# Optimization experiments

Hardware: AMD Instinct MI355X
Metric: run time of the kernel (lower is better)

## Reference

```python
import jax, jax.numpy as jnp
import numpy as np
import math

B, L, D, H = 4, 2048, 1024, 16
DH = D // H


def setup_inputs() -> dict:
    key = jax.random.key(0)
    ks = jax.random.split(key, 12)
    s = 0.02
    q = jax.random.normal(ks[0], (B, L, D), jnp.float32)
    k = jax.random.normal(ks[1], (B, L, D), jnp.float32)
    v = jax.random.normal(ks[2], (B, L, D), jnp.float32)
    # realistic padding: each sequence has a valid prefix of length in [L//2, L]
    lengths = jax.random.randint(ks[3], (B,), L // 2, L + 1)
    attention_mask = jnp.arange(L)[None, :] < lengths[:, None]  # [B, L] bool
    Wq = jax.random.normal(ks[4], (D, D), jnp.float32) * s
    bq = jnp.zeros((D,), jnp.float32)
    Wk = jax.random.normal(ks[5], (D, D), jnp.float32) * s
    bk = jnp.zeros((D,), jnp.float32)
    Wv = jax.random.normal(ks[6], (D, D), jnp.float32) * s
    bv = jnp.zeros((D,), jnp.float32)
    Wc = jax.random.normal(ks[7], (D, D), jnp.float32) * s
    bc = jnp.zeros((D,), jnp.float32)
    return {"q": q, "k": k, "v": v, "attention_mask": attention_mask,
            "Wq": Wq, "bq": bq, "Wk": Wk, "bk": bk,
            "Wv": Wv, "bv": bv, "Wc": Wc, "bc": bc}


def reference(q, k, v, attention_mask, Wq, bq, Wk, bk, Wv, bv, Wc, bc):
    b, l, d = q.shape
    # projections -> [B, H, L, DH]
    wq = (q @ Wq.T + bq).reshape(b, l, H, DH).transpose(0, 2, 1, 3)
    wk = (k @ Wk.T + bk).reshape(b, l, H, DH).transpose(0, 2, 1, 3)
    wv = (v @ Wv.T + bv).reshape(b, l, H, DH).transpose(0, 2, 1, 3)
    scores = jnp.einsum('bhqd,bhkd->bhqk', wq, wk) / math.sqrt(DH)  # [B,H,L,L]
    # fused causal + padding mask (additive, finfo.min like the torch code)
    pad2d = attention_mask[:, :, None] & attention_mask[:, None, :]  # [B,L,L]
    causal = jnp.tril(jnp.ones((l, l), dtype=bool))
    mask = pad2d[:, None, :, :] & causal[None, None, :, :]  # [B,1,L,L] -> broadcast over heads
    min_val = jnp.finfo(scores.dtype).min
    scores = scores + jnp.where(mask, jnp.float32(0.0), min_val).astype(scores.dtype)
    att = jax.nn.softmax(scores, axis=-1)
    out = jnp.einsum('bhqk,bhkd->bhqd', att, wv)  # [B,H,L,DH]
    out = out.transpose(0, 2, 1, 3).reshape(b, l, H * DH)
    return out @ Wc.T + bc
```

## Files before the change

### kernel.cpp

```cpp
#include <hip/hip_runtime.h>
#include <stdint.h>

typedef __bf16 bf16x8 __attribute__((ext_vector_type(8)));
typedef float f32x4 __attribute__((ext_vector_type(4)));
typedef unsigned short ushort8 __attribute__((ext_vector_type(8)));
typedef unsigned short ushort4v __attribute__((ext_vector_type(4)));

constexpr int CB = 4;
constexpr int CL = 2048;
constexpr int CD = 1024;
constexpr int CH = 16;
constexpr int CDH = 64;
constexpr int CM = CB * CL;

__device__ __forceinline__ unsigned short f2bf(float f) {
  union { float f; unsigned u; } x; x.f = f;
  unsigned r = x.u + 0x7fffu + ((x.u >> 16) & 1u);
  return (unsigned short)(r >> 16);
}
__device__ __forceinline__ float bf2f(unsigned short b) {
  union { unsigned u; float f; } x; x.u = ((unsigned)b) << 16;
  return x.f;
}

__device__ __forceinline__ void gld_lds16(const void* g, void* l) {
  __builtin_amdgcn_global_load_lds((const __attribute__((address_space(1))) void*)g,
                                   (__attribute__((address_space(3))) void*)l, 16, 0, 0);
}

#define MFMA16(a, b, c) __builtin_amdgcn_mfma_f32_16x16x32_bf16((a), (b), (c), 0, 0, 0)


__global__ __launch_bounds__(256) void cvt3_kernel(const float* __restrict__ q,
                                                   const float* __restrict__ k,
                                                   const float* __restrict__ v,
                                                   unsigned short* __restrict__ oq,
                                                   unsigned short* __restrict__ ok,
                                                   unsigned short* __restrict__ ov) {
  const int which = blockIdx.x >> 12;
  const int i = (blockIdx.x & 4095) * 256 + threadIdx.x;
  const float* s = which == 0 ? q : which == 1 ? k : v;
  unsigned short* d = which == 0 ? oq : which == 1 ? ok : ov;
  const float4* sp = (const float4*)s;
  float4 a = sp[2 * i], b = sp[2 * i + 1];
  ushort8 o;
  o[0] = f2bf(a.x); o[1] = f2bf(a.y); o[2] = f2bf(a.z); o[3] = f2bf(a.w);
  o[4] = f2bf(b.x); o[5] = f2bf(b.y); o[6] = f2bf(b.z); o[7] = f2bf(b.w);
  ((ushort8*)d)[i] = o;
}

__global__ __launch_bounds__(256) void cvtw_kernel(const float* w0, const float* w1,
                                                   const float* w2, const float* w3,
                                                   unsigned short* o0, unsigned short* o1,
                                                   unsigned short* o2, unsigned short* o3) {
  const int which = blockIdx.x >> 9;
  const int i = (blockIdx.x & 511) * 256 + threadIdx.x;
  const float* s = which == 0 ? w0 : which == 1 ? w1 : which == 2 ? w2 : w3;
  unsigned short* d = which == 0 ? o0 : which == 1 ? o1 : which == 2 ? o2 : o3;
  const float4* sp = (const float4*)s;
  float4 a = sp[2 * i], b = sp[2 * i + 1];
  ushort8 o;
  o[0] = f2bf(a.x); o[1] = f2bf(a.y); o[2] = f2bf(a.z); o[3] = f2bf(a.w);
  o[4] = f2bf(b.x); o[5] = f2bf(b.y); o[6] = f2bf(b.z); o[7] = f2bf(b.w);
  ((ushort8*)d)[i] = o;
}


__global__ __launch_bounds__(256) void lens_kernel(const int* __restrict__ mask,
                                                   int* __restrict__ lens) {
  __shared__ int part[4];
  const int b = blockIdx.x;
  int cnt = 0;
  for (int i = threadIdx.x; i < CL; i += 256) cnt += (mask[b * CL + i] != 0) ? 1 : 0;
#pragma unroll
  for (int off = 32; off; off >>= 1) cnt += __shfl_down(cnt, off);
  if ((threadIdx.x & 63) == 0) part[threadIdx.x >> 6] = cnt;
  __syncthreads();
  if (threadIdx.x == 0) lens[b] = part[0] + part[1] + part[2] + part[3];
}


__global__ __launch_bounds__(512) void gemm_qkv(const unsigned short* __restrict__ Xq,
                                                const unsigned short* __restrict__ Xk,
                                                const unsigned short* __restrict__ Xv,
                                                const unsigned short* __restrict__ Wb,
                                                const float* __restrict__ bq,
                                                const float* __restrict__ bk,
                                                const float* __restrict__ bv,
                                                unsigned short* __restrict__ Qp,
                                                unsigned short* __restrict__ Kp,
                                                unsigned short* __restrict__ Vt,
                                                float qscale) {
  __shared__ unsigned short Asm[2][128 * 32];
  __shared__ unsigned short Bsm[2][128 * 32];
  const int tid = threadIdx.x;
  const int w = tid >> 6, ln = tid & 63, lr = ln & 15, lq = ln >> 4;
  const int nbx = 24;
  const int cpx = (int)gridDim.x >> 3;
  const int bid = ((int)blockIdx.x & 7) * cpx + ((int)blockIdx.x >> 3);
  const int bm = (bid / nbx) << 7;
  const int bnG = (bid % nbx) << 7;
  const int which = bnG >> 10, bn = bnG & 1023;
  const unsigned short* A = which == 0 ? Xq : which == 1 ? Xk : Xv;
  const unsigned short* Bw = Wb + ((size_t)which << 20);
  const float* bias = which == 0 ? bq : which == 1 ? bk : bv;
  const float alpha = which == 0 ? qscale : 1.0f;
  const int wr = (w >> 1) << 5, wc = (w & 1) << 6;

  f32x4 acc[2][4] = {};
  const int arow = tid >> 2, akc = (tid & 3) << 3;

  auto stage = [&](int buf, int k0) {
    gld_lds16(A + (size_t)(bm + arow) * CD + k0 + akc, (void*)(Asm[buf] + w * 512));
    gld_lds16(Bw + (size_t)(bn + arow) * CD + k0 + akc, (void*)(Bsm[buf] + w * 512));
  };

  stage(0, 0);
  __syncthreads();

  const int nkt = CD >> 5;
  for (int kt = 0; kt < nkt; ++kt) {
    const int cur = kt & 1;
    if (kt + 1 < nkt) stage(cur ^ 1, (kt + 1) << 5);
    bf16x8 af[2], bfr[4];
#pragma unroll
    for (int f = 0; f < 2; ++f)
      af[f] = *(const bf16x8*)(Asm[cur] + ((wr + f * 16 + lr) * 32 + lq * 8));
#pragma unroll
    for (int f = 0; f < 4; ++f)
      bfr[f] = *(const bf16x8*)(Bsm[cur] + ((wc + f * 16 + lr) * 32 + lq * 8));
#pragma unroll
    for (int fm = 0; fm < 2; ++fm)
#pragma unroll
      for (int fn = 0; fn < 4; ++fn)
        acc[fm][fn] = MFMA16(af[fm], bfr[fn], acc[fm][fn]);
    __syncthreads();
  }

#pragma unroll
  for (int fm = 0; fm < 2; ++fm) {
    const int row0 = bm + wr + fm * 16 + lq * 4;
#pragma unroll
    for (int fn = 0; fn < 4; ++fn) {
      const int col = bn + wc + fn * 16 + lr;
      const float bb = bias[col];
      if (which == 2) {
        const int b = row0 >> 11, lrow = row0 & (CL - 1);
        const int hh = col >> 6, dh = col & 63;
        ushort4v pk;
#pragma unroll
        for (int j = 0; j < 4; ++j) pk[j] = f2bf(acc[fm][fn][j] + bb);
        *(ushort4v*)(Vt + (((size_t)((b * CH + hh) * CDH + dh)) << 11) + lrow) = pk;
      } else {
        unsigned short* outp = which == 0 ? Qp : Kp;
#pragma unroll
        for (int j = 0; j < 4; ++j)
          outp[(size_t)(row0 + j) * CD + col] = f2bf((acc[fm][fn][j] + bb) * alpha);
      }
    }
  }
}


__global__ __launch_bounds__(512) void gemm_out(const unsigned short* __restrict__ A,
                                                const unsigned short* __restrict__ Bw,
                                                const float* __restrict__ bias,
                                                float* __restrict__ Cout) {
  __shared__ unsigned short Asm[2][128 * 32];
  __shared__ unsigned short Bsm[2][128 * 32];
  const int tid = threadIdx.x;
  const int w = tid >> 6, ln = tid & 63, lr = ln & 15, lq = ln >> 4;
  const int nbx = CD >> 7;
  const int cpx = (int)gridDim.x >> 3;
  const int bid = ((int)blockIdx.x & 7) * cpx + ((int)blockIdx.x >> 3);
  const int bm = (bid / nbx) << 7;
  const int bn = (bid % nbx) << 7;
  const int wr = (w >> 1) << 5, wc = (w & 1) << 6;

  f32x4 acc[2][4] = {};
  const int arow = tid >> 2, akc = (tid & 3) << 3;

  auto stage = [&](int buf, int k0) {
    gld_lds16(A + (size_t)(bm + arow) * CD + k0 + akc, (void*)(Asm[buf] + w * 512));
    gld_lds16(Bw + (size_t)(bn + arow) * CD + k0 + akc, (void*)(Bsm[buf] + w * 512));
  };

  stage(0, 0);
  __syncthreads();

  const int nkt = CD >> 5;
  for (int kt = 0; kt < nkt; ++kt) {
    const int cur = kt & 1;
    if (kt + 1 < nkt) stage(cur ^ 1, (kt + 1) << 5);
    bf16x8 af[2], bfr[4];
#pragma unroll
    for (int f = 0; f < 2; ++f)
      af[f] = *(const bf16x8*)(Asm[cur] + ((wr + f * 16 + lr) * 32 + lq * 8));
#pragma unroll
    for (int f = 0; f < 4; ++f)
      bfr[f] = *(const bf16x8*)(Bsm[cur] + ((wc + f * 16 + lr) * 32 + lq * 8));
#pragma unroll
    for (int fm = 0; fm < 2; ++fm)
#pragma unroll
      for (int fn = 0; fn < 4; ++fn)
        acc[fm][fn] = MFMA16(af[fm], bfr[fn], acc[fm][fn]);
    __syncthreads();
  }

#pragma unroll
  for (int fm = 0; fm < 2; ++fm) {
    const int row0 = bm + wr + fm * 16 + lq * 4;
#pragma unroll
    for (int fn = 0; fn < 4; ++fn) {
      const int col = bn + wc + fn * 16 + lr;
      const float bb = bias[col];
#pragma unroll
      for (int j = 0; j < 4; ++j)
        Cout[(size_t)(row0 + j) * CD + col] = acc[fm][fn][j] + bb;
    }
  }
}


__global__ __launch_bounds__(256) void meanv_kernel(const unsigned short* __restrict__ Vt,
                                                    float* __restrict__ meanv) {
  const int row = blockIdx.x * 4 + (threadIdx.x >> 6);
  const int ln = threadIdx.x & 63;
  const ushort8* p = (const ushort8*)(Vt + (size_t)row * CL);
  float s = 0.f;
#pragma unroll
  for (int it = 0; it < 4; ++it) {
    ushort8 v = p[it * 64 + ln];
#pragma unroll
    for (int j = 0; j < 8; ++j) s += bf2f(v[j]);
  }
#pragma unroll
  for (int off = 32; off; off >>= 1) s += __shfl_down(s, off);
  if (ln == 0) meanv[row] = s * (1.f / (float)CL);
}


#define LOADK(kt, dst)                                                              \
  {                                                                                 \
    const int kb_ = (kt) << 6;                                                      \
    for (int cf_ = 0; cf_ < 4; ++cf_)                                               \
      for (int hf_ = 0; hf_ < 2; ++hf_)                                             \
        dst[cf_][hf_] = *(const bf16x8*)(Kbase + (size_t)(kb_ + cf_ * 16 + lr) * CD + \
                                         hf_ * 32 + lq * 8);                        \
  }

#define LOADV(kt, dst)                                                              \
  {                                                                                 \
    const int kb_ = (kt) << 6;                                                      \
    for (int df_ = 0; df_ < 4; ++df_)                                               \
      for (int hf_ = 0; hf_ < 2; ++hf_)                                             \
        dst[df_][hf_] = *(const bf16x8*)(Vbase + (((size_t)(df_ * 16 + lr)) << 11) +  \
                                         kb_ + hf_ * 32 + lq * 8);                  \
  }

#define TILE(kt, KF, KN)                                                            \
  {                                                                                 \
    const bool dm_ = (kt) == kdiag;                                                 \
    const int kb_ = (kt) << 6;                                                      \
    f32x4 s_[2][4];                                                                 \
    for (int rs_ = 0; rs_ < 2; ++rs_)                                               \
      for (int cf_ = 0; cf_ < 4; ++cf_) {                                           \
        f32x4 z_ = {};                                                              \
        z_ = MFMA16(qa[rs_][0], KF[cf_][0], z_);                                    \
        z_ = MFMA16(qa[rs_][1], KF[cf_][1], z_);                                    \
        s_[rs_][cf_] = z_;                                                          \
      }                                                                             \
    LOADV(kt, vb);                                                                  \
    if ((kt) < kdiag) LOADK((kt) + 1, KN);                                          \
    __builtin_amdgcn_sched_barrier(0);                                              \
    for (int rs_ = 0; rs_ < 2; ++rs_)                                               \
      for (int cf_ = 0; cf_ < 4; ++cf_)                                             \
        for (int j_ = 0; j_ < 4; ++j_) {                                            \
          float p_ = __builtin_amdgcn_exp2f(s_[rs_][cf_][j_]);                      \
          if (dm_) {                                                                \
            const int key_ = kb_ + cf_ * 16 + lr;                                   \
            const int row_ = rowbase + rs_ * 16 + lq * 4 + j_;                      \
            p_ = (key_ > row_) ? 0.f : p_;                                          \
          }                                                                         \
          lsum[rs_][j_] += p_;                                                      \
          Ps[rs_ * 16 + lq * 4 + j_][cf_ * 16 + lr] =                               \
              (unsigned short)(__builtin_bit_cast(unsigned int, p_) >> 16);         \
        }                                                                           \
    bf16x8 pa_[2][2];                                                               \
    for (int rs_ = 0; rs_ < 2; ++rs_)                                               \
      for (int hf_ = 0; hf_ < 2; ++hf_)                                             \
        pa_[rs_][hf_] = *(const bf16x8*)(&Ps[rs_ * 16 + lr][hf_ * 32 + lq * 8]);    \
    for (int df_ = 0; df_ < 4; ++df_) {                                             \
      o[0][df_] = MFMA16(pa_[0][0], vb[df_][0], o[0][df_]);                         \
      o[0][df_] = MFMA16(pa_[0][1], vb[df_][1], o[0][df_]);                         \
      o[1][df_] = MFMA16(pa_[1][0], vb[df_][0], o[1][df_]);                         \
      o[1][df_] = MFMA16(pa_[1][1], vb[df_][1], o[1][df_]);                         \
    }                                                                               \
  }

__global__ __launch_bounds__(64, 2) void attn_kernel(const unsigned short* __restrict__ Qp,
                                                     const unsigned short* __restrict__ Kp,
                                                     const unsigned short* __restrict__ Vt,
                                                     const int* __restrict__ lens,
                                                     unsigned short* __restrict__ attno) {
  __shared__ unsigned short Ps[32][72];
  const int i = blockIdx.x;
  const int xcd = i & 7, bh8 = (i >> 3) & 7, slot = i >> 6;
  const int qt = 15 - (slot >> 2), wv = slot & 3;
  const int bh = bh8 * 8 + xcd;
  const int b = bh >> 4, h = bh & 15;
  const int rowbase = (qt << 7) + (wv << 5);
  const int len = lens[b];
  if (rowbase >= len) return;

  const int tid = threadIdx.x, lr = tid & 15, lq = tid >> 4;

  const unsigned short* Kbase = Kp + (size_t)(b * CL) * CD + h * 64;
  const unsigned short* Vbase = Vt + ((size_t)(bh * 64) << 11);
  const unsigned short* Qbase = Qp + (size_t)(b * CL + rowbase) * CD + h * 64;

  bf16x8 qa[2][2];
#pragma unroll
  for (int rs = 0; rs < 2; ++rs)
#pragma unroll
    for (int hf = 0; hf < 2; ++hf)
      qa[rs][hf] = *(const bf16x8*)(Qbase + (size_t)(rs * 16 + lr) * CD + hf * 32 + lq * 8);

  f32x4 o[2][4] = {};
  float lsum[2][4] = {};
  const int kdiag = rowbase >> 6;

  bf16x8 kfA[4][2], kfB[4][2], vb[4][2];
  LOADK(0, kfA);

  int kt = 0;
  while (true) {
    TILE(kt, kfA, kfB);
    if (kt == kdiag) break;
    ++kt;
    TILE(kt, kfB, kfA);
    if (kt == kdiag) break;
    ++kt;
  }

  float inv[2][4];
#pragma unroll
  for (int rs = 0; rs < 2; ++rs)
#pragma unroll
    for (int j = 0; j < 4; ++j) {
      float t = lsum[rs][j];
      t += __shfl_xor(t, 1);
      t += __shfl_xor(t, 2);
      t += __shfl_xor(t, 4);
      t += __shfl_xor(t, 8);
      inv[rs][j] = __builtin_amdgcn_rcpf(t);
    }

#pragma unroll
  for (int rs = 0; rs < 2; ++rs)
#pragma unroll
    for (int df = 0; df < 4; ++df)
#pragma unroll
      for (int j = 0; j < 4; ++j)
        attno[(size_t)(b * CL + rowbase + rs * 16 + lq * 4 + j) * CD + h * 64 + df * 16 +
              lr] = f2bf(o[rs][df][j] * inv[rs][j]);
}


__global__ __launch_bounds__(256) void padfix_kernel(const int* __restrict__ lens,
                                                     const float* __restrict__ meanv,
                                                     unsigned short* __restrict__ attno) {
  const int q = blockIdx.x & (CL - 1);
  const int b = blockIdx.x >> 11;
  if (q < lens[b]) return;
#pragma unroll
  for (int i = 0; i < 4; ++i) {
    const int col = threadIdx.x + i * 256;
    attno[(size_t)(b * CL + q) * CD + col] = f2bf(meanv[b * CD + col]);
  }
}


extern "C" void kernel_launch(void* const* d_in, const int* in_sizes, int n_in,
                              void* d_out, int out_size, void* d_ws, size_t ws_size,
                              hipStream_t stream) {
  const float* q  = (const float*)d_in[0];
  const float* k  = (const float*)d_in[1];
  const float* v  = (const float*)d_in[2];
  const int*   am = (const int*)d_in[3];
  const float* Wq = (const float*)d_in[4];
  const float* bq = (const float*)d_in[5];
  const float* Wk = (const float*)d_in[6];
  const float* bk = (const float*)d_in[7];
  const float* Wv = (const float*)d_in[8];
  const float* bv = (const float*)d_in[9];
  const float* Wc = (const float*)d_in[10];
  const float* bc = (const float*)d_in[11];
  float* out = (float*)d_out;

  unsigned short* Wqb = (unsigned short*)d_ws;
  unsigned short* Wkb = Wqb + (1 << 20);
  unsigned short* Wvb = Wkb + (1 << 20);
  unsigned short* Wcb = Wvb + (1 << 20);
  unsigned short* Xq  = Wcb + (1 << 20);
  unsigned short* Xk  = Xq + (size_t)CM * CD;
  unsigned short* Xv  = Xk + (size_t)CM * CD;
  unsigned short* Qp  = Xv + (size_t)CM * CD;
  unsigned short* Kp  = Qp + (size_t)CM * CD;
  unsigned short* Vt  = Kp + (size_t)CM * CD;
  float* meanv = (float*)(Vt + (size_t)CM * CD);
  int* lens = (int*)(meanv + CB * CD);
  unsigned short* X = Xq;

  cvtw_kernel<<<2048, 256, 0, stream>>>(Wq, Wk, Wv, Wc, Wqb, Wkb, Wvb, Wcb);
  lens_kernel<<<CB, 256, 0, stream>>>(am, lens);
  cvt3_kernel<<<12288, 256, 0, stream>>>(q, k, v, Xq, Xk, Xv);

  const float QSCALE = 0.125f * 1.44269504f;

  gemm_qkv<<<1536, 512, 0, stream>>>(Xq, Xk, Xv, Wqb, bq, bk, bv, Qp, Kp, Vt, QSCALE);

  meanv_kernel<<<1024, 256, 0, stream>>>(Vt, meanv);

  attn_kernel<<<4096, 64, 0, stream>>>(Qp, Kp, Vt, lens, X);
  padfix_kernel<<<CB * CL, 256, 0, stream>>>(lens, meanv, X);

  gemm_out<<<512, 512, 0, stream>>>(X, Wcb, bc, out);
}
```

Baseline: 231.3 us.

## Split attention key tiles across four waves and pair causal query blocks

The attention kernel goes from one 64-thread wave per 32-row query block to 256-thread blocks. Each block handles a pair of query blocks (lo and hi), so causal work is balanced across blocks. Within a block the four waves stride over key tiles (kt += 4), and their partial outputs and row sums are merged through shared memory in a two-step reduction before wave 0 normalizes and writes. This targets load imbalance and the long serial key loop of late query blocks, at the cost of extra LDS traffic and several __syncthreads per half.

```diff
diff --git a/kernel.cpp b/kernel.cpp
--- a/kernel.cpp
+++ b/kernel.cpp
@@ -271,7 +271,7 @@
         s_[rs_][cf_] = z_;                                                          \
       }                                                                             \
     LOADV(kt, vb);                                                                  \
-    if ((kt) < kdiag) LOADK((kt) + 1, KN);                                          \
+    if ((kt) + 4 <= kdiag) LOADK((kt) + 4, KN);                                     \
     __builtin_amdgcn_sched_barrier(0);                                              \
     for (int rs_ = 0; rs_ < 2; ++rs_)                                               \
       for (int cf_ = 0; cf_ < 4; ++cf_)                                             \
@@ -283,13 +283,13 @@
             p_ = (key_ > row_) ? 0.f : p_;                                          \
           }                                                                         \
           lsum[rs_][j_] += p_;                                                      \
-          Ps[rs_ * 16 + lq * 4 + j_][cf_ * 16 + lr] =                               \
+          Psw[rs_ * 16 + lq * 4 + j_][cf_ * 16 + lr] =                              \
               (unsigned short)(__builtin_bit_cast(unsigned int, p_) >> 16);         \
         }                                                                           \
     bf16x8 pa_[2][2];                                                               \
     for (int rs_ = 0; rs_ < 2; ++rs_)                                               \
       for (int hf_ = 0; hf_ < 2; ++hf_)                                             \
-        pa_[rs_][hf_] = *(const bf16x8*)(&Ps[rs_ * 16 + lr][hf_ * 32 + lq * 8]);    \
+        pa_[rs_][hf_] = *(const bf16x8*)(&Psw[rs_ * 16 + lr][hf_ * 32 + lq * 8]);   \
     for (int df_ = 0; df_ < 4; ++df_) {                                             \
       o[0][df_] = MFMA16(pa_[0][0], vb[df_][0], o[0][df_]);                         \
       o[0][df_] = MFMA16(pa_[0][1], vb[df_][1], o[0][df_]);                         \
@@ -298,72 +298,150 @@
     }                                                                               \
   }
 
-__global__ __launch_bounds__(64, 2) void attn_kernel(const unsigned short* __restrict__ Qp,
-                                                     const unsigned short* __restrict__ Kp,
-                                                     const unsigned short* __restrict__ Vt,
-                                                     const int* __restrict__ lens,
-                                                     unsigned short* __restrict__ attno) {
-  __shared__ unsigned short Ps[32][72];
-  const int i = blockIdx.x;
-  const int xcd = i & 7, bh8 = (i >> 3) & 7, slot = i >> 6;
-  const int qt = 15 - (slot >> 2), wv = slot & 3;
-  const int bh = bh8 * 8 + xcd;
+__global__ __launch_bounds__(256, 2) void attn_kernel(const unsigned short* __restrict__ Qp,
+                                                      const unsigned short* __restrict__ Kp,
+                                                      const unsigned short* __restrict__ Vt,
+                                                      const int* __restrict__ lens,
+                                                      unsigned short* __restrict__ attno) {
+  __shared__ unsigned short Ps[4][32][72];
+  __shared__ float bufO[2][32][66];
+  __shared__ float bufL[2][2][16];
+  const int blk = blockIdx.x;
+  const int bh = (blk & 7) * 8 + ((blk >> 3) & 7);
+  const int p = blk >> 6;
   const int b = bh >> 4, h = bh & 15;
-  const int rowbase = (qt << 7) + (wv << 5);
   const int len = lens[b];
-  if (rowbase >= len) return;
-
-  const int tid = threadIdx.x, lr = tid & 15, lq = tid >> 4;
+  const int nvb = (len + 31) >> 5;
+  const int npair = (nvb + 1) >> 1;
+  if (p >= npair) return;
+  const int lo = p, hi = nvb - 1 - p;
+
+  const int tid = threadIdx.x, w = tid >> 6, lr = tid & 15, lq = (tid & 63) >> 4;
+  unsigned short (*Psw)[72] = Ps[w];
 
   const unsigned short* Kbase = Kp + (size_t)(b * CL) * CD + h * 64;
   const unsigned short* Vbase = Vt + ((size_t)(bh * 64) << 11);
-  const unsigned short* Qbase = Qp + (size_t)(b * CL + rowbase) * CD + h * 64;
-
-  bf16x8 qa[2][2];
-#pragma unroll
-  for (int rs = 0; rs < 2; ++rs)
-#pragma unroll
-    for (int hf = 0; hf < 2; ++hf)
-      qa[rs][hf] = *(const bf16x8*)(Qbase + (size_t)(rs * 16 + lr) * CD + hf * 32 + lq * 8);
-
-  f32x4 o[2][4] = {};
-  float lsum[2][4] = {};
-  const int kdiag = rowbase >> 6;
-
-  bf16x8 kfA[4][2], kfB[4][2], vb[4][2];
-  LOADK(0, kfA);
-
-  int kt = 0;
-  while (true) {
-    TILE(kt, kfA, kfB);
-    if (kt == kdiag) break;
-    ++kt;
-    TILE(kt, kfB, kfA);
-    if (kt == kdiag) break;
-    ++kt;
-  }
-
-  float inv[2][4];
-#pragma unroll
-  for (int rs = 0; rs < 2; ++rs)
-#pragma unroll
-    for (int j = 0; j < 4; ++j) {
-      float t = lsum[rs][j];
-      t += __shfl_xor(t, 1);
-      t += __shfl_xor(t, 2);
-      t += __shfl_xor(t, 4);
-      t += __shfl_xor(t, 8);
-      inv[rs][j] = __builtin_amdgcn_rcpf(t);
-    }
-
-#pragma unroll
-  for (int rs = 0; rs < 2; ++rs)
-#pragma unroll
-    for (int df = 0; df < 4; ++df)
-#pragma unroll
-      for (int j = 0; j < 4; ++j)
-        attno[(size_t)(b * CL + rowbase + rs * 16 + lq * 4 + j) * CD + h * 64 + df * 16 +
-              lr] = f2bf(o[rs][df][j] * inv[rs][j]);
+
+  auto half = [&](const int qb) {
+    const int rowbase = qb << 5;
+    const int kdiag = rowbase >> 6;
+    const unsigned short* Qbase = Qp + (size_t)(b * CL + rowbase) * CD + h * 64;
+
+    bf16x8 qa[2][2];
+#pragma unroll
+    for (int rs = 0; rs < 2; ++rs)
+#pragma unroll
+      for (int hf = 0; hf < 2; ++hf)
+        qa[rs][hf] =
+            *(const bf16x8*)(Qbase + (size_t)(rs * 16 + lr) * CD + hf * 32 + lq * 8);
+
+    f32x4 o[2][4] = {};
+    float lsum[2][4] = {};
+
+    bf16x8 kfA[4][2], kfB[4][2], vb[4][2];
+    int kt = w;
+    if (kt <= kdiag) {
+      LOADK(kt, kfA);
+      while (true) {
+        TILE(kt, kfA, kfB);
+        if (kt + 4 > kdiag) break;
+        kt += 4;
+        TILE(kt, kfB, kfA);
+        if (kt + 4 > kdiag) break;
+        kt += 4;
+      }
+    }
+
+#pragma unroll
+    for (int rs = 0; rs < 2; ++rs)
+#pragma unroll
+      for (int j = 0; j < 4; ++j) {
+        float t = lsum[rs][j];
+        t += __shfl_xor(t, 1);
+        t += __shfl_xor(t, 2);
+        t += __shfl_xor(t, 4);
+        t += __shfl_xor(t, 8);
+        lsum[rs][j] = t;
+      }
+
+    __syncthreads();
+    if (w == 1 || w == 3) {
+      const int buf = w >> 1;
+#pragma unroll
+      for (int rs = 0; rs < 2; ++rs)
+#pragma unroll
+        for (int df = 0; df < 4; ++df)
+#pragma unroll
+          for (int j = 0; j < 4; ++j)
+            bufO[buf][rs * 16 + lq * 4 + j][df * 16 + lr] = o[rs][df][j];
+      if (lr == 0) {
+#pragma unroll
+        for (int rs = 0; rs < 2; ++rs)
+#pragma unroll
+          for (int j = 0; j < 4; ++j) bufL[buf][rs][lq * 4 + j] = lsum[rs][j];
+      }
+    }
+    __syncthreads();
+    if (w == 0 || w == 2) {
+      const int buf = w >> 1;
+#pragma unroll
+      for (int rs = 0; rs < 2; ++rs)
+#pragma unroll
+        for (int df = 0; df < 4; ++df)
+#pragma unroll
+          for (int j = 0; j < 4; ++j)
+            o[rs][df][j] += bufO[buf][rs * 16 + lq * 4 + j][df * 16 + lr];
+#pragma unroll
+      for (int rs = 0; rs < 2; ++rs)
+#pragma unroll
+        for (int j = 0; j < 4; ++j) lsum[rs][j] += bufL[buf][rs][lq * 4 + j];
+    }
+    __syncthreads();
+    if (w == 2) {
+#pragma unroll
+      for (int rs = 0; rs < 2; ++rs)
+#pragma unroll
+        for (int df = 0; df < 4; ++df)
+#pragma unroll
+          for (int j = 0; j < 4; ++j)
+            bufO[0][rs * 16 + lq * 4 + j][df * 16 + lr] = o[rs][df][j];
+      if (lr == 0) {
+#pragma unroll
+        for (int rs = 0; rs < 2; ++rs)
+#pragma unroll
+          for (int j = 0; j < 4; ++j) bufL[0][rs][lq * 4 + j] = lsum[rs][j];
+      }
+    }
+    __syncthreads();
+    if (w == 0) {
+#pragma unroll
+      for (int rs = 0; rs < 2; ++rs) {
+#pragma unroll
+        for (int df = 0; df < 4; ++df)
+#pragma unroll
+          for (int j = 0; j < 4; ++j)
+            o[rs][df][j] += bufO[0][rs * 16 + lq * 4 + j][df * 16 + lr];
+#pragma unroll
+        for (int j = 0; j < 4; ++j) lsum[rs][j] += bufL[0][rs][lq * 4 + j];
+      }
+      float inv[2][4];
+#pragma unroll
+      for (int rs = 0; rs < 2; ++rs)
+#pragma unroll
+        for (int j = 0; j < 4; ++j) inv[rs][j] = __builtin_amdgcn_rcpf(lsum[rs][j]);
+#pragma unroll
+      for (int rs = 0; rs < 2; ++rs)
+#pragma unroll
+        for (int df = 0; df < 4; ++df)
+#pragma unroll
+          for (int j = 0; j < 4; ++j)
+            attno[(size_t)(b * CL + rowbase + rs * 16 + lq * 4 + j) * CD + h * 64 +
+                  df * 16 + lr] = f2bf(o[rs][df][j] * inv[rs][j]);
+    }
+  };
+
+  half(lo);
+  if (hi != lo) half(hi);
 }
 
 
@@ -422,7 +500,7 @@
 
   meanv_kernel<<<1024, 256, 0, stream>>>(Vt, meanv);
 
-  attn_kernel<<<4096, 64, 0, stream>>>(Qp, Kp, Vt, lens, X);
+  attn_kernel<<<2048, 256, 0, stream>>>(Qp, Kp, Vt, lens, X);
   padfix_kernel<<<CB * CL, 256, 0, stream>>>(lens, meanv, X);
 
   gemm_out<<<512, 512, 0, stream>>>(X, Wcb, bc, out);
```

Result: slower. 247.8 us (+7.1%).

## Fuse fp32-to-bf16 input conversion into QKV GEMM and software-pipeline attention tiles

Applied to the files above, without the earlier changes.

Drops the separate cvt3 kernel. The QKV GEMM now loads fp32 activations directly into registers, converts them to bf16, and writes them to LDS after the MFMAs, which removes a full read-write pass over the activations. Separately, the attention loop is restructured so the next tile's QK^T MFMAs and K/V loads overlap with the current tile's softmax and PV MFMAs. This hides latency at the cost of more registers. The GEMM A operand now goes through register staging instead of async global-to-LDS loads, which may expose load latency and doubles the global bytes the GEMM reads for A.

```diff
diff --git a/kernel.cpp b/kernel.cpp
--- a/kernel.cpp
+++ b/kernel.cpp
@@ -30,24 +30,6 @@
 
 #define MFMA16(a, b, c) __builtin_amdgcn_mfma_f32_16x16x32_bf16((a), (b), (c), 0, 0, 0)
 
-
-__global__ __launch_bounds__(256) void cvt3_kernel(const float* __restrict__ q,
-                                                   const float* __restrict__ k,
-                                                   const float* __restrict__ v,
-                                                   unsigned short* __restrict__ oq,
-                                                   unsigned short* __restrict__ ok,
-                                                   unsigned short* __restrict__ ov) {
-  const int which = blockIdx.x >> 12;
-  const int i = (blockIdx.x & 4095) * 256 + threadIdx.x;
-  const float* s = which == 0 ? q : which == 1 ? k : v;
-  unsigned short* d = which == 0 ? oq : which == 1 ? ok : ov;
-  const float4* sp = (const float4*)s;
-  float4 a = sp[2 * i], b = sp[2 * i + 1];
-  ushort8 o;
-  o[0] = f2bf(a.x); o[1] = f2bf(a.y); o[2] = f2bf(a.z); o[3] = f2bf(a.w);
-  o[4] = f2bf(b.x); o[5] = f2bf(b.y); o[6] = f2bf(b.z); o[7] = f2bf(b.w);
-  ((ushort8*)d)[i] = o;
-}
 
 __global__ __launch_bounds__(256) void cvtw_kernel(const float* w0, const float* w1,
                                                    const float* w2, const float* w3,
@@ -80,9 +62,9 @@
 }
 
 
-__global__ __launch_bounds__(512) void gemm_qkv(const unsigned short* __restrict__ Xq,
-                                                const unsigned short* __restrict__ Xk,
-                                                const unsigned short* __restrict__ Xv,
+__global__ __launch_bounds__(512) void gemm_qkv(const float* __restrict__ qf,
+                                                const float* __restrict__ kf,
+                                                const float* __restrict__ vf,
                                                 const unsigned short* __restrict__ Wb,
                                                 const float* __restrict__ bq,
                                                 const float* __restrict__ bk,
@@ -101,7 +83,7 @@
   const int bm = (bid / nbx) << 7;
   const int bnG = (bid % nbx) << 7;
   const int which = bnG >> 10, bn = bnG & 1023;
-  const unsigned short* A = which == 0 ? Xq : which == 1 ? Xk : Xv;
+  const float* Af = which == 0 ? qf : which == 1 ? kf : vf;
   const unsigned short* Bw = Wb + ((size_t)which << 20);
   const float* bias = which == 0 ? bq : which == 1 ? bk : bv;
   const float alpha = which == 0 ? qscale : 1.0f;
@@ -110,18 +92,35 @@
   f32x4 acc[2][4] = {};
   const int arow = tid >> 2, akc = (tid & 3) << 3;
 
-  auto stage = [&](int buf, int k0) {
-    gld_lds16(A + (size_t)(bm + arow) * CD + k0 + akc, (void*)(Asm[buf] + w * 512));
+  auto loadA = [&](int k0, float4& a0, float4& a1) {
+    const float* s = Af + (size_t)(bm + arow) * CD + k0 + akc;
+    a0 = *(const float4*)s;
+    a1 = *(const float4*)(s + 4);
+  };
+  auto writeA = [&](int buf, const float4& a0, const float4& a1) {
+    ushort8 o8;
+    o8[0] = f2bf(a0.x); o8[1] = f2bf(a0.y); o8[2] = f2bf(a0.z); o8[3] = f2bf(a0.w);
+    o8[4] = f2bf(a1.x); o8[5] = f2bf(a1.y); o8[6] = f2bf(a1.z); o8[7] = f2bf(a1.w);
+    *(ushort8*)(&Asm[buf][tid * 8]) = o8;
+  };
+  auto stageB = [&](int buf, int k0) {
     gld_lds16(Bw + (size_t)(bn + arow) * CD + k0 + akc, (void*)(Bsm[buf] + w * 512));
   };
 
-  stage(0, 0);
+  float4 a0, a1;
+  loadA(0, a0, a1);
+  stageB(0, 0);
+  writeA(0, a0, a1);
   __syncthreads();
 
   const int nkt = CD >> 5;
   for (int kt = 0; kt < nkt; ++kt) {
     const int cur = kt & 1;
-    if (kt + 1 < nkt) stage(cur ^ 1, (kt + 1) << 5);
+    const bool pre = kt + 1 < nkt;
+    if (pre) {
+      loadA((kt + 1) << 5, a0, a1);
+      stageB(cur ^ 1, (kt + 1) << 5);
+    }
     bf16x8 af[2], bfr[4];
 #pragma unroll
     for (int f = 0; f < 2; ++f)
@@ -134,6 +133,7 @@
 #pragma unroll
       for (int fn = 0; fn < 4; ++fn)
         acc[fm][fn] = MFMA16(af[fm], bfr[fn], acc[fm][fn]);
+    if (pre) writeA(cur ^ 1, a0, a1);
     __syncthreads();
   }
 
@@ -249,34 +249,34 @@
                                          hf_ * 32 + lq * 8);                        \
   }
 
-#define LOADV(kt, dst)                                                              \
+#define LOADV(kt)                                                                   \
   {                                                                                 \
     const int kb_ = (kt) << 6;                                                      \
     for (int df_ = 0; df_ < 4; ++df_)                                               \
       for (int hf_ = 0; hf_ < 2; ++hf_)                                             \
-        dst[df_][hf_] = *(const bf16x8*)(Vbase + (((size_t)(df_ * 16 + lr)) << 11) +  \
-                                         kb_ + hf_ * 32 + lq * 8);                  \
-  }
-
-#define TILE(kt, KF, KN)                                                            \
+        vb[df_][hf_] = *(const bf16x8*)(Vbase + (((size_t)(df_ * 16 + lr)) << 11) +   \
+                                        kb_ + hf_ * 32 + lq * 8);                   \
+  }
+
+#define QKT(KF)                                                                     \
   {                                                                                 \
-    const bool dm_ = (kt) == kdiag;                                                 \
-    const int kb_ = (kt) << 6;                                                      \
-    f32x4 s_[2][4];                                                                 \
     for (int rs_ = 0; rs_ < 2; ++rs_)                                               \
       for (int cf_ = 0; cf_ < 4; ++cf_) {                                           \
         f32x4 z_ = {};                                                              \
         z_ = MFMA16(qa[rs_][0], KF[cf_][0], z_);                                    \
         z_ = MFMA16(qa[rs_][1], KF[cf_][1], z_);                                    \
-        s_[rs_][cf_] = z_;                                                          \
+        s[rs_][cf_] = z_;                                                           \
       }                                                                             \
-    LOADV(kt, vb);                                                                  \
-    if ((kt) < kdiag) LOADK((kt) + 1, KN);                                          \
-    __builtin_amdgcn_sched_barrier(0);                                              \
+  }
+
+#define STAGE2(kt, KN, KL)                                                          \
+  {                                                                                 \
+    const bool dm_ = (kt) == kdiag;                                                 \
+    const int kb_ = (kt) << 6;                                                      \
     for (int rs_ = 0; rs_ < 2; ++rs_)                                               \
       for (int cf_ = 0; cf_ < 4; ++cf_)                                             \
         for (int j_ = 0; j_ < 4; ++j_) {                                            \
-          float p_ = __builtin_amdgcn_exp2f(s_[rs_][cf_][j_]);                      \
+          float p_ = __builtin_amdgcn_exp2f(s[rs_][cf_][j_]);                       \
           if (dm_) {                                                                \
             const int key_ = kb_ + cf_ * 16 + lr;                                   \
             const int row_ = rowbase + rs_ * 16 + lq * 4 + j_;                      \
@@ -290,12 +290,19 @@
     for (int rs_ = 0; rs_ < 2; ++rs_)                                               \
       for (int hf_ = 0; hf_ < 2; ++hf_)                                             \
         pa_[rs_][hf_] = *(const bf16x8*)(&Ps[rs_ * 16 + lr][hf_ * 32 + lq * 8]);    \
+    if ((kt) < kdiag) {                                                             \
+      QKT(KN);                   \
+      if ((kt) + 2 <= kdiag) LOADK((kt) + 2, KL);                                   \
+    }                                                                               \
+    __builtin_amdgcn_sched_barrier(0);                                              \
     for (int df_ = 0; df_ < 4; ++df_) {                                             \
       o[0][df_] = MFMA16(pa_[0][0], vb[df_][0], o[0][df_]);                         \
       o[0][df_] = MFMA16(pa_[0][1], vb[df_][1], o[0][df_]);                         \
       o[1][df_] = MFMA16(pa_[1][0], vb[df_][0], o[1][df_]);                         \
       o[1][df_] = MFMA16(pa_[1][1], vb[df_][1], o[1][df_]);                         \
     }                                                                               \
+    if ((kt) < kdiag) LOADV((kt) + 1);                                              \
+    __builtin_amdgcn_sched_barrier(0);                                              \
   }
 
 __global__ __launch_bounds__(64, 2) void attn_kernel(const unsigned short* __restrict__ Qp,
@@ -331,14 +338,20 @@
   const int kdiag = rowbase >> 6;
 
   bf16x8 kfA[4][2], kfB[4][2], vb[4][2];
+  f32x4 s[2][4];
+
   LOADK(0, kfA);
+  QKT(kfA);
+  LOADV(0);
+  if (kdiag > 0) LOADK(1, kfB);
+  __builtin_amdgcn_sched_barrier(0);
 
   int kt = 0;
   while (true) {
-    TILE(kt, kfA, kfB);
+    STAGE2(kt, kfB, kfA);
     if (kt == kdiag) break;
     ++kt;
-    TILE(kt, kfB, kfA);
+    STAGE2(kt, kfA, kfB);
     if (kt == kdiag) break;
     ++kt;
   }
@@ -402,23 +415,19 @@
   unsigned short* Wkb = Wqb + (1 << 20);
   unsigned short* Wvb = Wkb + (1 << 20);
   unsigned short* Wcb = Wvb + (1 << 20);
-  unsigned short* Xq  = Wcb + (1 << 20);
-  unsigned short* Xk  = Xq + (size_t)CM * CD;
-  unsigned short* Xv  = Xk + (size_t)CM * CD;
-  unsigned short* Qp  = Xv + (size_t)CM * CD;
+  unsigned short* X   = Wcb + (1 << 20);
+  unsigned short* Qp  = X  + (size_t)CM * CD;
   unsigned short* Kp  = Qp + (size_t)CM * CD;
   unsigned short* Vt  = Kp + (size_t)CM * CD;
   float* meanv = (float*)(Vt + (size_t)CM * CD);
   int* lens = (int*)(meanv + CB * CD);
-  unsigned short* X = Xq;
 
   cvtw_kernel<<<2048, 256, 0, stream>>>(Wq, Wk, Wv, Wc, Wqb, Wkb, Wvb, Wcb);
   lens_kernel<<<CB, 256, 0, stream>>>(am, lens);
-  cvt3_kernel<<<12288, 256, 0, stream>>>(q, k, v, Xq, Xk, Xv);
 
   const float QSCALE = 0.125f * 1.44269504f;
 
-  gemm_qkv<<<1536, 512, 0, stream>>>(Xq, Xk, Xv, Wqb, bq, bk, bv, Qp, Kp, Vt, QSCALE);
+  gemm_qkv<<<1536, 512, 0, stream>>>(q, k, v, Wqb, bq, bk, bv, Qp, Kp, Vt, QSCALE);
 
   meanv_kernel<<<1024, 256, 0, stream>>>(Vt, meanv);
 
```

Measured after the change: 253.6 us. 1.1x slower.

## Software-pipeline attention loop: overlap next QK^T with current PV

Applied to the files above, without the earlier changes.

Restructures the attention inner loop so the QK^T MFMAs for the next key tile are issued before the PV MFMAs of the current tile, while K is prefetched two tiles ahead and V one tile ahead. The aim is to hide the exp/softmax ALU work and global-load latency behind matrix-core work. The cost is higher register pressure from the extra in-flight score buffer and K prefetch, which could hurt occupancy at launch bounds (64,2).

```diff
diff --git a/kernel.cpp b/kernel.cpp
--- a/kernel.cpp
+++ b/kernel.cpp
@@ -249,34 +249,34 @@
                                          hf_ * 32 + lq * 8);                        \
   }
 
-#define LOADV(kt, dst)                                                              \
+#define LOADV(kt)                                                                   \
   {                                                                                 \
     const int kb_ = (kt) << 6;                                                      \
     for (int df_ = 0; df_ < 4; ++df_)                                               \
       for (int hf_ = 0; hf_ < 2; ++hf_)                                             \
-        dst[df_][hf_] = *(const bf16x8*)(Vbase + (((size_t)(df_ * 16 + lr)) << 11) +  \
-                                         kb_ + hf_ * 32 + lq * 8);                  \
-  }
-
-#define TILE(kt, KF, KN)                                                            \
+        vb[df_][hf_] = *(const bf16x8*)(Vbase + (((size_t)(df_ * 16 + lr)) << 11) +   \
+                                        kb_ + hf_ * 32 + lq * 8);                   \
+  }
+
+#define QKT(KF)                                                                     \
   {                                                                                 \
-    const bool dm_ = (kt) == kdiag;                                                 \
-    const int kb_ = (kt) << 6;                                                      \
-    f32x4 s_[2][4];                                                                 \
     for (int rs_ = 0; rs_ < 2; ++rs_)                                               \
       for (int cf_ = 0; cf_ < 4; ++cf_) {                                           \
         f32x4 z_ = {};                                                              \
         z_ = MFMA16(qa[rs_][0], KF[cf_][0], z_);                                    \
         z_ = MFMA16(qa[rs_][1], KF[cf_][1], z_);                                    \
-        s_[rs_][cf_] = z_;                                                          \
+        s[rs_][cf_] = z_;                                                           \
       }                                                                             \
-    LOADV(kt, vb);                                                                  \
-    if ((kt) < kdiag) LOADK((kt) + 1, KN);                                          \
-    __builtin_amdgcn_sched_barrier(0);                                              \
+  }
+
+#define STAGE2(kt, KN, KL)                                                          \
+  {                                                                                 \
+    const bool dm_ = (kt) == kdiag;                                                 \
+    const int kb_ = (kt) << 6;                                                      \
     for (int rs_ = 0; rs_ < 2; ++rs_)                                               \
       for (int cf_ = 0; cf_ < 4; ++cf_)                                             \
         for (int j_ = 0; j_ < 4; ++j_) {                                            \
-          float p_ = __builtin_amdgcn_exp2f(s_[rs_][cf_][j_]);                      \
+          float p_ = __builtin_amdgcn_exp2f(s[rs_][cf_][j_]);                       \
           if (dm_) {                                                                \
             const int key_ = kb_ + cf_ * 16 + lr;                                   \
             const int row_ = rowbase + rs_ * 16 + lq * 4 + j_;                      \
@@ -290,12 +290,19 @@
     for (int rs_ = 0; rs_ < 2; ++rs_)                                               \
       for (int hf_ = 0; hf_ < 2; ++hf_)                                             \
         pa_[rs_][hf_] = *(const bf16x8*)(&Ps[rs_ * 16 + lr][hf_ * 32 + lq * 8]);    \
+    if ((kt) < kdiag) {                                                             \
+      QKT(KN);                   \
+      if ((kt) + 2 <= kdiag) LOADK((kt) + 2, KL);                                   \
+    }                                                                               \
+    __builtin_amdgcn_sched_barrier(0);                                              \
     for (int df_ = 0; df_ < 4; ++df_) {                                             \
       o[0][df_] = MFMA16(pa_[0][0], vb[df_][0], o[0][df_]);                         \
       o[0][df_] = MFMA16(pa_[0][1], vb[df_][1], o[0][df_]);                         \
       o[1][df_] = MFMA16(pa_[1][0], vb[df_][0], o[1][df_]);                         \
       o[1][df_] = MFMA16(pa_[1][1], vb[df_][1], o[1][df_]);                         \
     }                                                                               \
+    if ((kt) < kdiag) LOADV((kt) + 1);                                              \
+    __builtin_amdgcn_sched_barrier(0);                                              \
   }
 
 __global__ __launch_bounds__(64, 2) void attn_kernel(const unsigned short* __restrict__ Qp,
@@ -331,14 +338,20 @@
   const int kdiag = rowbase >> 6;
 
   bf16x8 kfA[4][2], kfB[4][2], vb[4][2];
+  f32x4 s[2][4];
+
   LOADK(0, kfA);
+  QKT(kfA);
+  LOADV(0);
+  if (kdiag > 0) LOADK(1, kfB);
+  __builtin_amdgcn_sched_barrier(0);
 
   int kt = 0;
   while (true) {
-    TILE(kt, kfA, kfB);
+    STAGE2(kt, kfB, kfA);
     if (kt == kdiag) break;
     ++kt;
-    TILE(kt, kfB, kfA);
+    STAGE2(kt, kfA, kfB);
     if (kt == kdiag) break;
     ++kt;
   }
```

New measurement: 263.1 us. 13.7% more time.
